# Kernel optimization log

Hardware: AMD Instinct MI355X
Metric: run time of the kernel (lower is better)

## Reference

```python
import jax, jax.numpy as jnp
import numpy as np

VOCAB = 100000
EMBED = 128
HIDDEN = 256
N_TRIPLES = 1_000_000


def setup_inputs() -> dict:
    key = jax.random.key(0)
    ks = jax.random.split(key, 12)

    def xavier(k, fan_in, fan_out):
        limit = float(np.sqrt(6.0 / (fan_in + fan_out)))
        return jax.random.uniform(k, (fan_in, fan_out), jnp.float32, -limit, limit)

    triples = jax.random.randint(ks[0], (N_TRIPLES, 3), 0, VOCAB, dtype=jnp.int32)
    entity_table = jax.random.normal(ks[1], (VOCAB, EMBED), jnp.float32) * 0.02
    relation_table = jax.random.normal(ks[2], (VOCAB, EMBED), jnp.float32) * 0.02
    return {
        "triples": triples,
        "entity_table": entity_table,
        "relation_table": relation_table,
        "W1": xavier(ks[3], 3 * EMBED, HIDDEN), "b1": jnp.zeros((HIDDEN,), jnp.float32),
        "W2": xavier(ks[4], HIDDEN, HIDDEN),    "b2": jnp.zeros((HIDDEN,), jnp.float32),
        "W3": xavier(ks[5], HIDDEN, EMBED),     "b3": jnp.zeros((EMBED,), jnp.float32),
        "Wf1": xavier(ks[6], EMBED, HIDDEN),    "bf1": jnp.zeros((HIDDEN,), jnp.float32),
        "Wf2": xavier(ks[7], HIDDEN, EMBED),    "bf2": jnp.zeros((EMBED,), jnp.float32),
    }


def reference(triples, entity_table, relation_table,
              W1, b1, W2, b2, W3, b3, Wf1, bf1, Wf2, bf2):
    # Batched gather: [N, embed] each
    e1 = entity_table[triples[:, 0]]
    rel = relation_table[triples[:, 1]]
    e2 = entity_table[triples[:, 2]]
    x = jnp.concatenate([e1, rel, e2], axis=-1)  # [N, 3*embed]
    # graph_encoder: Linear-ReLU-Linear-ReLU-Linear
    h = jax.nn.relu(x @ W1 + b1)
    h = jax.nn.relu(h @ W2 + b2)
    enc = h @ W3 + b3                            # [N, embed]
    agg = jnp.mean(enc, axis=0)                  # [embed]
    # final_encoder: Linear-ReLU-Linear
    out = jax.nn.relu(agg @ Wf1 + bf1) @ Wf2 + bf2
    return out
```

## Files before the change

### kernel.cpp

```cpp
#include <hip/hip_runtime.h>
#include <hip/hip_bf16.h>


#define EMBED 128
#define BM 64
#define NBUCKET 128

typedef __bf16 bf16x8 __attribute__((ext_vector_type(8)));
typedef __bf16 bf16x4 __attribute__((ext_vector_type(4)));
typedef float f32x4 __attribute__((ext_vector_type(4)));

__global__ void pack_cvt(const float* __restrict__ src, __bf16* __restrict__ dst,
                         int K, int N) {
    int e = blockIdx.x * 256 + threadIdx.x;
    if (e >= K * N) return;
    int j = e & 7;
    int l = (e >> 3) & 63;
    int tile = e >> 9;
    int KT = K >> 5;
    int kt = tile % KT;
    int mt = tile / KT;
    int k = kt * 32 + (l >> 4) * 8 + j;
    int nc = mt * 16 + (l & 15);
    dst[e] = (__bf16)src[k * N + nc];
}

__global__ __launch_bounds__(256, 3) void mlp_main(
    const int* __restrict__ triples,
    const float* __restrict__ ent, const float* __restrict__ rel,
    const __bf16* __restrict__ W1p, const float* __restrict__ b1,
    const __bf16* __restrict__ W2p, const float* __restrict__ b2,
    const __bf16* __restrict__ W3p,
    float* __restrict__ part, int n)
{
    __shared__ unsigned char lds[49152];
    unsigned char* xs  = lds;
    unsigned char* h1s = lds;
    unsigned char* h2s = lds;

    const int tid  = threadIdx.x;
    const int wave = tid >> 6;
    const int lane = tid & 63;
    const int l15  = lane & 15;
    const int l4   = lane >> 4;
    const int s0   = blockIdx.x * BM;
    const int sp   = tid >> 4;
    const int ch   = tid & 15;

    int rows[3][4];
#pragma unroll
    for (int p = 0; p < 4; p++) {
        int g = s0 + p * 16 + sp;
        const int* t = triples + (g < n ? g : 0) * 3;
        rows[0][p] = t[0]; rows[1][p] = t[1]; rows[2][p] = t[2];
    }
    float4 ga[3][4], gb[3][4];
#pragma unroll
    for (int c = 0; c < 3; c++) {
        const float* tbl = (c == 1) ? rel : ent;
#pragma unroll
        for (int p = 0; p < 4; p++) {
            const float* src = tbl + (long)rows[c][p] * EMBED + ch * 8;
            ga[c][p] = *(const float4*)src;
            gb[c][p] = *(const float4*)(src + 4);
        }
    }
#pragma unroll
    for (int c = 0; c < 3; c++)
#pragma unroll
        for (int p = 0; p < 4; p++) {
            bf16x8 w;
            w[0] = (__bf16)ga[c][p].x; w[1] = (__bf16)ga[c][p].y;
            w[2] = (__bf16)ga[c][p].z; w[3] = (__bf16)ga[c][p].w;
            w[4] = (__bf16)gb[c][p].x; w[5] = (__bf16)gb[c][p].y;
            w[6] = (__bf16)gb[c][p].z; w[7] = (__bf16)gb[c][p].w;
            int s = p * 16 + sp;
            int off = (s * 768 + c * 256 + ch * 16) ^ ((s & 7) << 4);
            *(bf16x8*)(xs + off) = w;
        }
    __syncthreads();

    f32x4 acc[4][4];
    {
        const int fb = wave * 64;
#pragma unroll
        for (int m = 0; m < 4; m++) {
            f32x4 bias = *(const f32x4*)(b1 + fb + m * 16 + l4 * 4);
#pragma unroll
            for (int nn = 0; nn < 4; nn++) acc[m][nn] = bias;
        }
    }
    __builtin_amdgcn_s_setprio(1);
#pragma unroll
    for (int kk = 0; kk < 12; kk++) {
        bf16x8 bfr[4];
#pragma unroll
        for (int nn = 0; nn < 4; nn++) {
            int s = nn * 16 + l15;
            int off = (s * 768 + kk * 64 + l4 * 16) ^ ((s & 7) << 4);
            bfr[nn] = *(const bf16x8*)(xs + off);
        }
        bf16x8 afr[4];
#pragma unroll
        for (int m = 0; m < 4; m++)
            afr[m] = *(const bf16x8*)(W1p + ((wave * 4 + m) * 12 + kk) * 512 + lane * 8);
#pragma unroll
        for (int m = 0; m < 4; m++)
#pragma unroll
            for (int nn = 0; nn < 4; nn++)
                acc[m][nn] = __builtin_amdgcn_mfma_f32_16x16x32_bf16(
                    afr[m], bfr[nn], acc[m][nn], 0, 0, 0);
    }
    __builtin_amdgcn_s_setprio(0);
    __syncthreads();
#pragma unroll
    for (int m = 0; m < 4; m++) {
        int f0 = wave * 64 + m * 16 + l4 * 4;
#pragma unroll
        for (int nn = 0; nn < 4; nn++) {
            int s = nn * 16 + l15;
            bf16x4 p;
#pragma unroll
            for (int j = 0; j < 4; j++) {
                float v = acc[m][nn][j];
                p[j] = (__bf16)(v > 0.f ? v : 0.f);
            }
            int off = (s * 512 + f0 * 2) ^ ((s & 7) << 4);
            *(bf16x4*)(h1s + off) = p;
        }
    }
    __syncthreads();

    f32x4 acc2[4][4];
    {
        const int fb = wave * 64;
#pragma unroll
        for (int m = 0; m < 4; m++) {
            f32x4 bias = *(const f32x4*)(b2 + fb + m * 16 + l4 * 4);
#pragma unroll
            for (int nn = 0; nn < 4; nn++) acc2[m][nn] = bias;
        }
    }
    __builtin_amdgcn_s_setprio(1);
#pragma unroll
    for (int kk = 0; kk < 8; kk++) {
        bf16x8 bfr[4];
#pragma unroll
        for (int nn = 0; nn < 4; nn++) {
            int s = nn * 16 + l15;
            int off = (s * 512 + kk * 64 + l4 * 16) ^ ((s & 7) << 4);
            bfr[nn] = *(const bf16x8*)(h1s + off);
        }
        bf16x8 afr[4];
#pragma unroll
        for (int m = 0; m < 4; m++)
            afr[m] = *(const bf16x8*)(W2p + ((wave * 4 + m) * 8 + kk) * 512 + lane * 8);
#pragma unroll
        for (int m = 0; m < 4; m++)
#pragma unroll
            for (int nn = 0; nn < 4; nn++)
                acc2[m][nn] = __builtin_amdgcn_mfma_f32_16x16x32_bf16(
                    afr[m], bfr[nn], acc2[m][nn], 0, 0, 0);
    }
    __builtin_amdgcn_s_setprio(0);
    __syncthreads();
#pragma unroll
    for (int m = 0; m < 4; m++) {
        int f0 = wave * 64 + m * 16 + l4 * 4;
#pragma unroll
        for (int nn = 0; nn < 4; nn++) {
            int s = nn * 16 + l15;
            bf16x4 p;
#pragma unroll
            for (int j = 0; j < 4; j++) {
                float v = acc2[m][nn][j];
                p[j] = (__bf16)(v > 0.f ? v : 0.f);
            }
            int off = (s * 512 + f0 * 2) ^ ((s & 7) << 4);
            *(bf16x4*)(h2s + off) = p;
        }
    }
    __syncthreads();

    f32x4 acc3[2][4];
#pragma unroll
    for (int m = 0; m < 2; m++)
#pragma unroll
        for (int nn = 0; nn < 4; nn++)
            acc3[m][nn] = (f32x4)(0.f);
    __builtin_amdgcn_s_setprio(1);
#pragma unroll
    for (int kk = 0; kk < 8; kk++) {
        bf16x8 bfr[4];
#pragma unroll
        for (int nn = 0; nn < 4; nn++) {
            int s = nn * 16 + l15;
            int off = (s * 512 + kk * 64 + l4 * 16) ^ ((s & 7) << 4);
            bfr[nn] = *(const bf16x8*)(h2s + off);
        }
        bf16x8 afr[2];
#pragma unroll
        for (int m = 0; m < 2; m++)
            afr[m] = *(const bf16x8*)(W3p + ((wave * 2 + m) * 8 + kk) * 512 + lane * 8);
#pragma unroll
        for (int m = 0; m < 2; m++)
#pragma unroll
            for (int nn = 0; nn < 4; nn++)
                acc3[m][nn] = __builtin_amdgcn_mfma_f32_16x16x32_bf16(
                    afr[m], bfr[nn], acc3[m][nn], 0, 0, 0);
    }
    __builtin_amdgcn_s_setprio(0);
    {
        float* bucket = part + (blockIdx.x & (NBUCKET - 1)) * 128;
#pragma unroll
        for (int m = 0; m < 2; m++) {
#pragma unroll
            for (int j = 0; j < 4; j++) {
                float v = 0.f;
#pragma unroll
                for (int nn = 0; nn < 4; nn++) {
                    int g = s0 + nn * 16 + l15;
                    float t = acc3[m][nn][j];
                    v += (g < n) ? t : 0.f;
                }
                for (int off = 1; off < 16; off <<= 1) v += __shfl_xor(v, off);
                if (l15 == 0) {
                    int f = wave * 32 + m * 16 + l4 * 4 + j;
                    atomicAdd(bucket + f, v);
                }
            }
        }
    }
}

__global__ void head_kernel(const float* __restrict__ part, const float* __restrict__ b3,
                            const float* __restrict__ Wf1, const float* __restrict__ bf1,
                            const float* __restrict__ Wf2, const float* __restrict__ bf2,
                            float* __restrict__ out, int n)
{
    __shared__ float agg[128];
    __shared__ float t[256];
    const int tid = threadIdx.x;
    if (tid < 128) {
        float s = 0.f;
        for (int b = 0; b < NBUCKET; b++) s += part[b * 128 + tid];
        agg[tid] = s / (float)n + b3[tid];
    }
    __syncthreads();
    {
        float a = bf1[tid];
        for (int k = 0; k < 128; k++) a += agg[k] * Wf1[k * 256 + tid];
        t[tid] = a > 0.f ? a : 0.f;
    }
    __syncthreads();
    if (tid < 128) {
        float o = bf2[tid];
        for (int i = 0; i < 256; i++) o += t[i] * Wf2[i * 128 + tid];
        out[tid] = o;
    }
}

extern "C" void kernel_launch(void* const* d_in, const int* in_sizes, int n_in,
                              void* d_out, int out_size, void* d_ws, size_t ws_size,
                              hipStream_t stream) {
    const int*   triples = (const int*)d_in[0];
    const float* ent     = (const float*)d_in[1];
    const float* rel     = (const float*)d_in[2];
    const float* W1      = (const float*)d_in[3];
    const float* b1      = (const float*)d_in[4];
    const float* W2      = (const float*)d_in[5];
    const float* b2      = (const float*)d_in[6];
    const float* W3      = (const float*)d_in[7];
    const float* b3      = (const float*)d_in[8];
    const float* Wf1     = (const float*)d_in[9];
    const float* bf1     = (const float*)d_in[10];
    const float* Wf2     = (const float*)d_in[11];
    const float* bf2     = (const float*)d_in[12];
    float* out = (float*)d_out;
    const int n = in_sizes[0] / 3;

    __bf16* W1p = (__bf16*)d_ws;
    __bf16* W2p = (__bf16*)((char*)d_ws + 196608);
    __bf16* W3p = (__bf16*)((char*)d_ws + 327680);
    float*  prt = (float*)((char*)d_ws + 393216);

    pack_cvt<<<(384 * 256 + 255) / 256, 256, 0, stream>>>(W1, W1p, 384, 256);
    pack_cvt<<<(256 * 256 + 255) / 256, 256, 0, stream>>>(W2, W2p, 256, 256);
    pack_cvt<<<(256 * 128 + 255) / 256, 256, 0, stream>>>(W3, W3p, 256, 128);
    hipMemsetAsync(prt, 0, NBUCKET * 128 * sizeof(float), stream);

    const int blocks = (n + BM - 1) / BM;
    mlp_main<<<blocks, 256, 0, stream>>>(triples, ent, rel, W1p, b1, W2p, b2, W3p, prt, n);
    head_kernel<<<1, 256, 0, stream>>>(prt, b3, Wf1, bf1, Wf2, bf2, out, n);
}
```

Measured before the change: 508.2 us.

## Switch MLP GEMMs to 32x32x16 MFMA and fuse weight prep launches

Replaces the 16x16x32 bf16 MFMA tiling in all three encoder layers with 32x32x16 MFMA tiles. The weight packing layout, accumulator layout, bias initialisation, ReLU writeback and final reduction are all reworked to match. The three pack kernels and the memset are merged into a single prep launch. The larger MFMA tiles need fewer LDS fragment loads per FLOP, at the cost of different register pressure and reduction shuffles.

```diff
diff --git a/kernel.cpp b/kernel.cpp
--- a/kernel.cpp
+++ b/kernel.cpp
@@ -9,19 +9,24 @@
 typedef __bf16 bf16x8 __attribute__((ext_vector_type(8)));
 typedef __bf16 bf16x4 __attribute__((ext_vector_type(4)));
 typedef float f32x4 __attribute__((ext_vector_type(4)));
-
-__global__ void pack_cvt(const float* __restrict__ src, __bf16* __restrict__ dst,
-                         int K, int N) {
-    int e = blockIdx.x * 256 + threadIdx.x;
-    if (e >= K * N) return;
-    int j = e & 7;
-    int l = (e >> 3) & 63;
-    int tile = e >> 9;
-    int KT = K >> 5;
-    int kt = tile % KT;
-    int mt = tile / KT;
-    int k = kt * 32 + (l >> 4) * 8 + j;
-    int nc = mt * 16 + (l & 15);
+typedef float f32x16 __attribute__((ext_vector_type(16)));
+
+__global__ void prep_all(const float* __restrict__ W1, const float* __restrict__ W2,
+                         const float* __restrict__ W3,
+                         __bf16* __restrict__ W1p, __bf16* __restrict__ W2p,
+                         __bf16* __restrict__ W3p, float* __restrict__ prt) {
+    int idx = blockIdx.x * 256 + threadIdx.x;
+    if (idx < NBUCKET * 128) prt[idx] = 0.f;
+    const float* src; __bf16* dst; int K, N, e;
+    if (idx < 98304)       { src = W1; dst = W1p; K = 384; N = 256; e = idx; }
+    else if (idx < 163840) { src = W2; dst = W2p; K = 256; N = 256; e = idx - 98304; }
+    else if (idx < 196608) { src = W3; dst = W3p; K = 256; N = 128; e = idx - 163840; }
+    else return;
+    int j = e & 7, l = (e >> 3) & 63, t = e >> 9;
+    int KT = K >> 4;
+    int kt = t % KT, mt = t / KT;
+    int k  = kt * 16 + (l >> 5) * 8 + j;
+    int nc = mt * 32 + (l & 31);
     dst[e] = (__bf16)src[k * N + nc];
 }
 
@@ -41,8 +46,9 @@
     const int tid  = threadIdx.x;
     const int wave = tid >> 6;
     const int lane = tid & 63;
-    const int l15  = lane & 15;
-    const int l4   = lane >> 4;
+    const int l31  = lane & 31;
+    const int hi   = lane >> 5;
+    const int swzB = (l31 & 7) << 4;
     const int s0   = blockIdx.x * BM;
     const int sp   = tid >> 4;
     const int ch   = tid & 15;
@@ -80,154 +86,147 @@
         }
     __syncthreads();
 
-    f32x4 acc[4][4];
-    {
-        const int fb = wave * 64;
-#pragma unroll
-        for (int m = 0; m < 4; m++) {
-            f32x4 bias = *(const f32x4*)(b1 + fb + m * 16 + l4 * 4);
-#pragma unroll
-            for (int nn = 0; nn < 4; nn++) acc[m][nn] = bias;
-        }
-    }
+    f32x16 acc[2][2];
+#pragma unroll
+    for (int m = 0; m < 2; m++)
+#pragma unroll
+        for (int g = 0; g < 4; g++) {
+            f32x4 bb = *(const f32x4*)(b1 + wave * 64 + m * 32 + g * 8 + hi * 4);
+#pragma unroll
+            for (int nn = 0; nn < 2; nn++)
+#pragma unroll
+                for (int j = 0; j < 4; j++) acc[m][nn][g * 4 + j] = bb[j];
+        }
     __builtin_amdgcn_s_setprio(1);
 #pragma unroll
-    for (int kk = 0; kk < 12; kk++) {
-        bf16x8 bfr[4];
-#pragma unroll
-        for (int nn = 0; nn < 4; nn++) {
-            int s = nn * 16 + l15;
-            int off = (s * 768 + kk * 64 + l4 * 16) ^ ((s & 7) << 4);
-            bfr[nn] = *(const bf16x8*)(xs + off);
-        }
-        bf16x8 afr[4];
-#pragma unroll
-        for (int m = 0; m < 4; m++)
-            afr[m] = *(const bf16x8*)(W1p + ((wave * 4 + m) * 12 + kk) * 512 + lane * 8);
-#pragma unroll
-        for (int m = 0; m < 4; m++)
-#pragma unroll
-            for (int nn = 0; nn < 4; nn++)
-                acc[m][nn] = __builtin_amdgcn_mfma_f32_16x16x32_bf16(
+    for (int kk = 0; kk < 24; kk++) {
+        bf16x8 bfr[2];
+#pragma unroll
+        for (int nn = 0; nn < 2; nn++) {
+            int s = nn * 32 + l31;
+            bfr[nn] = *(const bf16x8*)(xs + ((s * 768 + kk * 32 + hi * 16) ^ swzB));
+        }
+        bf16x8 afr[2];
+#pragma unroll
+        for (int m = 0; m < 2; m++)
+            afr[m] = *(const bf16x8*)(W1p + ((wave * 2 + m) * 24 + kk) * 512 + lane * 8);
+#pragma unroll
+        for (int m = 0; m < 2; m++)
+#pragma unroll
+            for (int nn = 0; nn < 2; nn++)
+                acc[m][nn] = __builtin_amdgcn_mfma_f32_32x32x16_bf16(
                     afr[m], bfr[nn], acc[m][nn], 0, 0, 0);
     }
     __builtin_amdgcn_s_setprio(0);
     __syncthreads();
 #pragma unroll
-    for (int m = 0; m < 4; m++) {
-        int f0 = wave * 64 + m * 16 + l4 * 4;
-#pragma unroll
-        for (int nn = 0; nn < 4; nn++) {
-            int s = nn * 16 + l15;
-            bf16x4 p;
-#pragma unroll
-            for (int j = 0; j < 4; j++) {
-                float v = acc[m][nn][j];
-                p[j] = (__bf16)(v > 0.f ? v : 0.f);
-            }
-            int off = (s * 512 + f0 * 2) ^ ((s & 7) << 4);
-            *(bf16x4*)(h1s + off) = p;
-        }
-    }
-    __syncthreads();
-
-    f32x4 acc2[4][4];
-    {
-        const int fb = wave * 64;
-#pragma unroll
-        for (int m = 0; m < 4; m++) {
-            f32x4 bias = *(const f32x4*)(b2 + fb + m * 16 + l4 * 4);
-#pragma unroll
-            for (int nn = 0; nn < 4; nn++) acc2[m][nn] = bias;
-        }
-    }
+    for (int m = 0; m < 2; m++)
+#pragma unroll
+        for (int nn = 0; nn < 2; nn++) {
+            int s = nn * 32 + l31;
+#pragma unroll
+            for (int g = 0; g < 4; g++) {
+                int f0 = wave * 64 + m * 32 + g * 8 + hi * 4;
+                bf16x4 p;
+#pragma unroll
+                for (int j = 0; j < 4; j++) {
+                    float v = acc[m][nn][g * 4 + j];
+                    p[j] = (__bf16)(v > 0.f ? v : 0.f);
+                }
+                *(bf16x4*)(h1s + ((s * 512 + f0 * 2) ^ ((s & 7) << 4))) = p;
+            }
+        }
+    __syncthreads();
+
+    f32x16 acc2[2][2];
+#pragma unroll
+    for (int m = 0; m < 2; m++)
+#pragma unroll
+        for (int g = 0; g < 4; g++) {
+            f32x4 bb = *(const f32x4*)(b2 + wave * 64 + m * 32 + g * 8 + hi * 4);
+#pragma unroll
+            for (int nn = 0; nn < 2; nn++)
+#pragma unroll
+                for (int j = 0; j < 4; j++) acc2[m][nn][g * 4 + j] = bb[j];
+        }
     __builtin_amdgcn_s_setprio(1);
 #pragma unroll
-    for (int kk = 0; kk < 8; kk++) {
-        bf16x8 bfr[4];
-#pragma unroll
-        for (int nn = 0; nn < 4; nn++) {
-            int s = nn * 16 + l15;
-            int off = (s * 512 + kk * 64 + l4 * 16) ^ ((s & 7) << 4);
-            bfr[nn] = *(const bf16x8*)(h1s + off);
-        }
-        bf16x8 afr[4];
-#pragma unroll
-        for (int m = 0; m < 4; m++)
-            afr[m] = *(const bf16x8*)(W2p + ((wave * 4 + m) * 8 + kk) * 512 + lane * 8);
-#pragma unroll
-        for (int m = 0; m < 4; m++)
-#pragma unroll
-            for (int nn = 0; nn < 4; nn++)
-                acc2[m][nn] = __builtin_amdgcn_mfma_f32_16x16x32_bf16(
+    for (int kk = 0; kk < 16; kk++) {
+        bf16x8 bfr[2];
+#pragma unroll
+        for (int nn = 0; nn < 2; nn++) {
+            int s = nn * 32 + l31;
+            bfr[nn] = *(const bf16x8*)(h1s + ((s * 512 + kk * 32 + hi * 16) ^ swzB));
+        }
+        bf16x8 afr[2];
+#pragma unroll
+        for (int m = 0; m < 2; m++)
+            afr[m] = *(const bf16x8*)(W2p + ((wave * 2 + m) * 16 + kk) * 512 + lane * 8);
+#pragma unroll
+        for (int m = 0; m < 2; m++)
+#pragma unroll
+            for (int nn = 0; nn < 2; nn++)
+                acc2[m][nn] = __builtin_amdgcn_mfma_f32_32x32x16_bf16(
                     afr[m], bfr[nn], acc2[m][nn], 0, 0, 0);
     }
     __builtin_amdgcn_s_setprio(0);
     __syncthreads();
 #pragma unroll
-    for (int m = 0; m < 4; m++) {
-        int f0 = wave * 64 + m * 16 + l4 * 4;
-#pragma unroll
-        for (int nn = 0; nn < 4; nn++) {
-            int s = nn * 16 + l15;
-            bf16x4 p;
-#pragma unroll
-            for (int j = 0; j < 4; j++) {
-                float v = acc2[m][nn][j];
-                p[j] = (__bf16)(v > 0.f ? v : 0.f);
-            }
-            int off = (s * 512 + f0 * 2) ^ ((s & 7) << 4);
-            *(bf16x4*)(h2s + off) = p;
-        }
-    }
-    __syncthreads();
-
-    f32x4 acc3[2][4];
-#pragma unroll
-    for (int m = 0; m < 2; m++)
-#pragma unroll
-        for (int nn = 0; nn < 4; nn++)
-            acc3[m][nn] = (f32x4)(0.f);
+    for (int m = 0; m < 2; m++)
+#pragma unroll
+        for (int nn = 0; nn < 2; nn++) {
+            int s = nn * 32 + l31;
+#pragma unroll
+            for (int g = 0; g < 4; g++) {
+                int f0 = wave * 64 + m * 32 + g * 8 + hi * 4;
+                bf16x4 p;
+#pragma unroll
+                for (int j = 0; j < 4; j++) {
+                    float v = acc2[m][nn][g * 4 + j];
+                    p[j] = (__bf16)(v > 0.f ? v : 0.f);
+                }
+                *(bf16x4*)(h2s + ((s * 512 + f0 * 2) ^ ((s & 7) << 4))) = p;
+            }
+        }
+    __syncthreads();
+
+    f32x16 acc3[2];
+#pragma unroll
+    for (int nn = 0; nn < 2; nn++)
+#pragma unroll
+        for (int j = 0; j < 16; j++) acc3[nn][j] = 0.f;
     __builtin_amdgcn_s_setprio(1);
 #pragma unroll
-    for (int kk = 0; kk < 8; kk++) {
-        bf16x8 bfr[4];
-#pragma unroll
-        for (int nn = 0; nn < 4; nn++) {
-            int s = nn * 16 + l15;
-            int off = (s * 512 + kk * 64 + l4 * 16) ^ ((s & 7) << 4);
-            bfr[nn] = *(const bf16x8*)(h2s + off);
-        }
-        bf16x8 afr[2];
-#pragma unroll
-        for (int m = 0; m < 2; m++)
-            afr[m] = *(const bf16x8*)(W3p + ((wave * 2 + m) * 8 + kk) * 512 + lane * 8);
-#pragma unroll
-        for (int m = 0; m < 2; m++)
-#pragma unroll
-            for (int nn = 0; nn < 4; nn++)
-                acc3[m][nn] = __builtin_amdgcn_mfma_f32_16x16x32_bf16(
-                    afr[m], bfr[nn], acc3[m][nn], 0, 0, 0);
+    for (int kk = 0; kk < 16; kk++) {
+        bf16x8 afr = *(const bf16x8*)(W3p + (wave * 16 + kk) * 512 + lane * 8);
+#pragma unroll
+        for (int nn = 0; nn < 2; nn++) {
+            int s = nn * 32 + l31;
+            bf16x8 bfr = *(const bf16x8*)(h2s + ((s * 512 + kk * 32 + hi * 16) ^ swzB));
+            acc3[nn] = __builtin_amdgcn_mfma_f32_32x32x16_bf16(
+                afr, bfr, acc3[nn], 0, 0, 0);
+        }
     }
     __builtin_amdgcn_s_setprio(0);
     {
         float* bucket = part + (blockIdx.x & (NBUCKET - 1)) * 128;
 #pragma unroll
-        for (int m = 0; m < 2; m++) {
-#pragma unroll
-            for (int j = 0; j < 4; j++) {
-                float v = 0.f;
-#pragma unroll
-                for (int nn = 0; nn < 4; nn++) {
-                    int g = s0 + nn * 16 + l15;
-                    float t = acc3[m][nn][j];
-                    v += (g < n) ? t : 0.f;
-                }
-                for (int off = 1; off < 16; off <<= 1) v += __shfl_xor(v, off);
-                if (l15 == 0) {
-                    int f = wave * 32 + m * 16 + l4 * 4 + j;
-                    atomicAdd(bucket + f, v);
-                }
+        for (int r = 0; r < 16; r++) {
+            float v = 0.f;
+#pragma unroll
+            for (int nn = 0; nn < 2; nn++) {
+                int g = s0 + nn * 32 + l31;
+                float t = acc3[nn][r];
+                v += (g < n) ? t : 0.f;
+            }
+            v += __shfl_xor(v, 1);
+            v += __shfl_xor(v, 2);
+            v += __shfl_xor(v, 4);
+            v += __shfl_xor(v, 8);
+            v += __shfl_xor(v, 16);
+            if (l31 == 0) {
+                int f = wave * 32 + (r & 3) + 8 * (r >> 2) + hi * 4;
+                atomicAdd(bucket + f, v);
             }
         }
     }
@@ -284,10 +283,7 @@
     __bf16* W3p = (__bf16*)((char*)d_ws + 327680);
     float*  prt = (float*)((char*)d_ws + 393216);
 
-    pack_cvt<<<(384 * 256 + 255) / 256, 256, 0, stream>>>(W1, W1p, 384, 256);
-    pack_cvt<<<(256 * 256 + 255) / 256, 256, 0, stream>>>(W2, W2p, 256, 256);
-    pack_cvt<<<(256 * 128 + 255) / 256, 256, 0, stream>>>(W3, W3p, 256, 128);
-    hipMemsetAsync(prt, 0, NBUCKET * 128 * sizeof(float), stream);
+    prep_all<<<768, 256, 0, stream>>>(W1, W2, W3, W1p, W2p, W3p, prt);
 
     const int blocks = (n + BM - 1) / BM;
     mlp_main<<<blocks, 256, 0, stream>>>(triples, ent, rel, W1p, b1, W2p, b2, W3p, prt, n);
```

After: 539.2 us. 6.1% more time.

## Split layer-1 K loop to shrink LDS and merge weight prep launches

Applied to the files above, without the earlier changes.

The X tile in LDS drops from 48KB to 32KB by staging only e1 and rel first. The e2 gather is issued into registers during the first 8 K-steps, then written over the e1 region for the last 4 K-steps. This lets launch bounds rise from 3 to 4 blocks per CU. Separately, the three weight pack kernels and the memset are merged into one prep launch to cut launch overhead. The cost is an extra barrier pair, plus extra live registers for the prefetched gather under a tighter register budget.

```diff
diff --git a/kernel.cpp b/kernel.cpp
--- a/kernel.cpp
+++ b/kernel.cpp
@@ -10,22 +10,26 @@
 typedef __bf16 bf16x4 __attribute__((ext_vector_type(4)));
 typedef float f32x4 __attribute__((ext_vector_type(4)));
 
-__global__ void pack_cvt(const float* __restrict__ src, __bf16* __restrict__ dst,
-                         int K, int N) {
-    int e = blockIdx.x * 256 + threadIdx.x;
-    if (e >= K * N) return;
-    int j = e & 7;
-    int l = (e >> 3) & 63;
-    int tile = e >> 9;
+__global__ void prep_all(const float* __restrict__ W1, const float* __restrict__ W2,
+                         const float* __restrict__ W3,
+                         __bf16* __restrict__ W1p, __bf16* __restrict__ W2p,
+                         __bf16* __restrict__ W3p, float* __restrict__ prt) {
+    int idx = blockIdx.x * 256 + threadIdx.x;
+    if (idx < NBUCKET * 128) prt[idx] = 0.f;
+    const float* src; __bf16* dst; int K, N, e;
+    if (idx < 98304)       { src = W1; dst = W1p; K = 384; N = 256; e = idx; }
+    else if (idx < 163840) { src = W2; dst = W2p; K = 256; N = 256; e = idx - 98304; }
+    else if (idx < 196608) { src = W3; dst = W3p; K = 256; N = 128; e = idx - 163840; }
+    else return;
+    int j = e & 7, l = (e >> 3) & 63, t = e >> 9;
     int KT = K >> 5;
-    int kt = tile % KT;
-    int mt = tile / KT;
-    int k = kt * 32 + (l >> 4) * 8 + j;
+    int kt = t % KT, mt = t / KT;
+    int k  = kt * 32 + (l >> 4) * 8 + j;
     int nc = mt * 16 + (l & 15);
     dst[e] = (__bf16)src[k * N + nc];
 }
 
-__global__ __launch_bounds__(256, 3) void mlp_main(
+__global__ __launch_bounds__(256, 4) void mlp_main(
     const int* __restrict__ triples,
     const float* __restrict__ ent, const float* __restrict__ rel,
     const __bf16* __restrict__ W1p, const float* __restrict__ b1,
@@ -33,8 +37,7 @@
     const __bf16* __restrict__ W3p,
     float* __restrict__ part, int n)
 {
-    __shared__ unsigned char lds[49152];
-    unsigned char* xs  = lds;
+    __shared__ unsigned char lds[32768];
     unsigned char* h1s = lds;
     unsigned char* h2s = lds;
 
@@ -54,9 +57,9 @@
         const int* t = triples + (g < n ? g : 0) * 3;
         rows[0][p] = t[0]; rows[1][p] = t[1]; rows[2][p] = t[2];
     }
-    float4 ga[3][4], gb[3][4];
-#pragma unroll
-    for (int c = 0; c < 3; c++) {
+    float4 ga[2][4], gb[2][4];
+#pragma unroll
+    for (int c = 0; c < 2; c++) {
         const float* tbl = (c == 1) ? rel : ent;
 #pragma unroll
         for (int p = 0; p < 4; p++) {
@@ -66,7 +69,7 @@
         }
     }
 #pragma unroll
-    for (int c = 0; c < 3; c++)
+    for (int c = 0; c < 2; c++)
 #pragma unroll
         for (int p = 0; p < 4; p++) {
             bf16x8 w;
@@ -75,10 +78,18 @@
             w[4] = (__bf16)gb[c][p].x; w[5] = (__bf16)gb[c][p].y;
             w[6] = (__bf16)gb[c][p].z; w[7] = (__bf16)gb[c][p].w;
             int s = p * 16 + sp;
-            int off = (s * 768 + c * 256 + ch * 16) ^ ((s & 7) << 4);
-            *(bf16x8*)(xs + off) = w;
-        }
-    __syncthreads();
+            int off = c * 16384 + ((s * 256 + ch * 16) ^ ((s & 7) << 4));
+            *(bf16x8*)(lds + off) = w;
+        }
+    __syncthreads();
+
+    float4 g2a[4], g2b[4];
+#pragma unroll
+    for (int p = 0; p < 4; p++) {
+        const float* src = ent + (long)rows[2][p] * EMBED + ch * 8;
+        g2a[p] = *(const float4*)src;
+        g2b[p] = *(const float4*)(src + 4);
+    }
 
     f32x4 acc[4][4];
     {
@@ -92,13 +103,49 @@
     }
     __builtin_amdgcn_s_setprio(1);
 #pragma unroll
-    for (int kk = 0; kk < 12; kk++) {
+    for (int kk = 0; kk < 8; kk++) {
         bf16x8 bfr[4];
 #pragma unroll
         for (int nn = 0; nn < 4; nn++) {
             int s = nn * 16 + l15;
-            int off = (s * 768 + kk * 64 + l4 * 16) ^ ((s & 7) << 4);
-            bfr[nn] = *(const bf16x8*)(xs + off);
+            int off = (kk >> 2) * 16384 +
+                      ((s * 256 + (kk & 3) * 64 + l4 * 16) ^ ((s & 7) << 4));
+            bfr[nn] = *(const bf16x8*)(lds + off);
+        }
+        bf16x8 afr[4];
+#pragma unroll
+        for (int m = 0; m < 4; m++)
+            afr[m] = *(const bf16x8*)(W1p + ((wave * 4 + m) * 12 + kk) * 512 + lane * 8);
+#pragma unroll
+        for (int m = 0; m < 4; m++)
+#pragma unroll
+            for (int nn = 0; nn < 4; nn++)
+                acc[m][nn] = __builtin_amdgcn_mfma_f32_16x16x32_bf16(
+                    afr[m], bfr[nn], acc[m][nn], 0, 0, 0);
+    }
+    __builtin_amdgcn_s_setprio(0);
+    __syncthreads();
+#pragma unroll
+    for (int p = 0; p < 4; p++) {
+        bf16x8 w;
+        w[0] = (__bf16)g2a[p].x; w[1] = (__bf16)g2a[p].y;
+        w[2] = (__bf16)g2a[p].z; w[3] = (__bf16)g2a[p].w;
+        w[4] = (__bf16)g2b[p].x; w[5] = (__bf16)g2b[p].y;
+        w[6] = (__bf16)g2b[p].z; w[7] = (__bf16)g2b[p].w;
+        int s = p * 16 + sp;
+        int off = (s * 256 + ch * 16) ^ ((s & 7) << 4);
+        *(bf16x8*)(lds + off) = w;
+    }
+    __syncthreads();
+    __builtin_amdgcn_s_setprio(1);
+#pragma unroll
+    for (int kk = 8; kk < 12; kk++) {
+        bf16x8 bfr[4];
+#pragma unroll
+        for (int nn = 0; nn < 4; nn++) {
+            int s = nn * 16 + l15;
+            int off = (s * 256 + (kk & 3) * 64 + l4 * 16) ^ ((s & 7) << 4);
+            bfr[nn] = *(const bf16x8*)(lds + off);
         }
         bf16x8 afr[4];
 #pragma unroll
@@ -284,10 +331,7 @@
     __bf16* W3p = (__bf16*)((char*)d_ws + 327680);
     float*  prt = (float*)((char*)d_ws + 393216);
 
-    pack_cvt<<<(384 * 256 + 255) / 256, 256, 0, stream>>>(W1, W1p, 384, 256);
-    pack_cvt<<<(256 * 256 + 255) / 256, 256, 0, stream>>>(W2, W2p, 256, 256);
-    pack_cvt<<<(256 * 128 + 255) / 256, 256, 0, stream>>>(W3, W3p, 256, 128);
-    hipMemsetAsync(prt, 0, NBUCKET * 128 * sizeof(float), stream);
+    prep_all<<<768, 256, 0, stream>>>(W1, W2, W3, W1p, W2p, W3p, prt);
 
     const int blocks = (n + BM - 1) / BM;
     mlp_main<<<blocks, 256, 0, stream>>>(triples, ent, rel, W1p, b1, W2p, b2, W3p, prt, n);
```

After: 862.1 us. 69.6% more time.

## Split MLP block work across 8 waves and fuse weight-prep launches

Applied to the files above, without the earlier changes.

Doubles the mlp_main block to 512 threads (8 waves), so each wave computes half as many output-feature tiles per layer. The gather is restructured so each thread loads one row segment of 16 floats per table. The three weight pack kernels and the memset are merged into a single prep kernel to cut launch overhead. The goal is more waves in flight to hide gather latency and lower per-wave register pressure. The cost is that each B fragment read from LDS is now reused by fewer MFMAs, which raises LDS traffic per flop.

```diff
diff --git a/kernel.cpp b/kernel.cpp
--- a/kernel.cpp
+++ b/kernel.cpp
@@ -10,22 +10,26 @@
 typedef __bf16 bf16x4 __attribute__((ext_vector_type(4)));
 typedef float f32x4 __attribute__((ext_vector_type(4)));
 
-__global__ void pack_cvt(const float* __restrict__ src, __bf16* __restrict__ dst,
-                         int K, int N) {
-    int e = blockIdx.x * 256 + threadIdx.x;
-    if (e >= K * N) return;
-    int j = e & 7;
-    int l = (e >> 3) & 63;
-    int tile = e >> 9;
+__global__ void prep_all(const float* __restrict__ W1, const float* __restrict__ W2,
+                         const float* __restrict__ W3,
+                         __bf16* __restrict__ W1p, __bf16* __restrict__ W2p,
+                         __bf16* __restrict__ W3p, float* __restrict__ prt) {
+    int idx = blockIdx.x * 256 + threadIdx.x;
+    if (idx < NBUCKET * 128) prt[idx] = 0.f;
+    const float* src; __bf16* dst; int K, N, e;
+    if (idx < 98304)       { src = W1; dst = W1p; K = 384; N = 256; e = idx; }
+    else if (idx < 163840) { src = W2; dst = W2p; K = 256; N = 256; e = idx - 98304; }
+    else if (idx < 196608) { src = W3; dst = W3p; K = 256; N = 128; e = idx - 163840; }
+    else return;
+    int j = e & 7, l = (e >> 3) & 63, t = e >> 9;
     int KT = K >> 5;
-    int kt = tile % KT;
-    int mt = tile / KT;
-    int k = kt * 32 + (l >> 4) * 8 + j;
+    int kt = t % KT, mt = t / KT;
+    int k  = kt * 32 + (l >> 4) * 8 + j;
     int nc = mt * 16 + (l & 15);
     dst[e] = (__bf16)src[k * N + nc];
 }
 
-__global__ __launch_bounds__(256, 3) void mlp_main(
+__global__ __launch_bounds__(512, 6) void mlp_main(
     const int* __restrict__ triples,
     const float* __restrict__ ent, const float* __restrict__ rel,
     const __bf16* __restrict__ W1p, const float* __restrict__ b1,
@@ -44,51 +48,43 @@
     const int l15  = lane & 15;
     const int l4   = lane >> 4;
     const int s0   = blockIdx.x * BM;
-    const int sp   = tid >> 4;
-    const int ch   = tid & 15;
-
-    int rows[3][4];
-#pragma unroll
-    for (int p = 0; p < 4; p++) {
-        int g = s0 + p * 16 + sp;
-        const int* t = triples + (g < n ? g : 0) * 3;
-        rows[0][p] = t[0]; rows[1][p] = t[1]; rows[2][p] = t[2];
-    }
-    float4 ga[3][4], gb[3][4];
-#pragma unroll
-    for (int c = 0; c < 3; c++) {
-        const float* tbl = (c == 1) ? rel : ent;
-#pragma unroll
-        for (int p = 0; p < 4; p++) {
-            const float* src = tbl + (long)rows[c][p] * EMBED + ch * 8;
-            ga[c][p] = *(const float4*)src;
-            gb[c][p] = *(const float4*)(src + 4);
-        }
-    }
-#pragma unroll
-    for (int c = 0; c < 3; c++)
-#pragma unroll
-        for (int p = 0; p < 4; p++) {
-            bf16x8 w;
-            w[0] = (__bf16)ga[c][p].x; w[1] = (__bf16)ga[c][p].y;
-            w[2] = (__bf16)ga[c][p].z; w[3] = (__bf16)ga[c][p].w;
-            w[4] = (__bf16)gb[c][p].x; w[5] = (__bf16)gb[c][p].y;
-            w[6] = (__bf16)gb[c][p].z; w[7] = (__bf16)gb[c][p].w;
-            int s = p * 16 + sp;
-            int off = (s * 768 + c * 256 + ch * 16) ^ ((s & 7) << 4);
-            *(bf16x8*)(xs + off) = w;
-        }
-    __syncthreads();
-
-    f32x4 acc[4][4];
+    const int sg   = tid >> 3;
+    const int q    = tid & 7;
+
     {
-        const int fb = wave * 64;
-#pragma unroll
-        for (int m = 0; m < 4; m++) {
-            f32x4 bias = *(const f32x4*)(b1 + fb + m * 16 + l4 * 4);
-#pragma unroll
-            for (int nn = 0; nn < 4; nn++) acc[m][nn] = bias;
-        }
+        int g = s0 + sg;
+        const int* tp = triples + (g < n ? g : 0) * 3;
+#pragma unroll
+        for (int c = 0; c < 3; c++) {
+            const float* tbl = (c == 1) ? rel : ent;
+            const float* src = tbl + (long)tp[c] * EMBED + q * 16;
+            float4 v0 = *(const float4*)(src);
+            float4 v1 = *(const float4*)(src + 4);
+            float4 v2 = *(const float4*)(src + 8);
+            float4 v3 = *(const float4*)(src + 12);
+            bf16x8 w0, w1;
+            w0[0] = (__bf16)v0.x; w0[1] = (__bf16)v0.y;
+            w0[2] = (__bf16)v0.z; w0[3] = (__bf16)v0.w;
+            w0[4] = (__bf16)v1.x; w0[5] = (__bf16)v1.y;
+            w0[6] = (__bf16)v1.z; w0[7] = (__bf16)v1.w;
+            w1[0] = (__bf16)v2.x; w1[1] = (__bf16)v2.y;
+            w1[2] = (__bf16)v2.z; w1[3] = (__bf16)v2.w;
+            w1[4] = (__bf16)v3.x; w1[5] = (__bf16)v3.y;
+            w1[6] = (__bf16)v3.z; w1[7] = (__bf16)v3.w;
+            int base = sg * 768 + c * 256 + q * 32;
+            int swz  = (sg & 7) << 4;
+            *(bf16x8*)(xs + (base ^ swz))        = w0;
+            *(bf16x8*)(xs + ((base + 16) ^ swz)) = w1;
+        }
+    }
+    __syncthreads();
+
+    f32x4 acc[2][4];
+#pragma unroll
+    for (int m = 0; m < 2; m++) {
+        f32x4 bias = *(const f32x4*)(b1 + wave * 32 + m * 16 + l4 * 4);
+#pragma unroll
+        for (int nn = 0; nn < 4; nn++) acc[m][nn] = bias;
     }
     __builtin_amdgcn_s_setprio(1);
 #pragma unroll
@@ -100,12 +96,12 @@
             int off = (s * 768 + kk * 64 + l4 * 16) ^ ((s & 7) << 4);
             bfr[nn] = *(const bf16x8*)(xs + off);
         }
-        bf16x8 afr[4];
-#pragma unroll
-        for (int m = 0; m < 4; m++)
-            afr[m] = *(const bf16x8*)(W1p + ((wave * 4 + m) * 12 + kk) * 512 + lane * 8);
-#pragma unroll
-        for (int m = 0; m < 4; m++)
+        bf16x8 afr[2];
+#pragma unroll
+        for (int m = 0; m < 2; m++)
+            afr[m] = *(const bf16x8*)(W1p + ((wave * 2 + m) * 12 + kk) * 512 + lane * 8);
+#pragma unroll
+        for (int m = 0; m < 2; m++)
 #pragma unroll
             for (int nn = 0; nn < 4; nn++)
                 acc[m][nn] = __builtin_amdgcn_mfma_f32_16x16x32_bf16(
@@ -114,8 +110,8 @@
     __builtin_amdgcn_s_setprio(0);
     __syncthreads();
 #pragma unroll
-    for (int m = 0; m < 4; m++) {
-        int f0 = wave * 64 + m * 16 + l4 * 4;
+    for (int m = 0; m < 2; m++) {
+        int f0 = wave * 32 + m * 16 + l4 * 4;
 #pragma unroll
         for (int nn = 0; nn < 4; nn++) {
             int s = nn * 16 + l15;
@@ -131,15 +127,12 @@
     }
     __syncthreads();
 
-    f32x4 acc2[4][4];
-    {
-        const int fb = wave * 64;
-#pragma unroll
-        for (int m = 0; m < 4; m++) {
-            f32x4 bias = *(const f32x4*)(b2 + fb + m * 16 + l4 * 4);
-#pragma unroll
-            for (int nn = 0; nn < 4; nn++) acc2[m][nn] = bias;
-        }
+    f32x4 acc2[2][4];
+#pragma unroll
+    for (int m = 0; m < 2; m++) {
+        f32x4 bias = *(const f32x4*)(b2 + wave * 32 + m * 16 + l4 * 4);
+#pragma unroll
+        for (int nn = 0; nn < 4; nn++) acc2[m][nn] = bias;
     }
     __builtin_amdgcn_s_setprio(1);
 #pragma unroll
@@ -151,12 +144,12 @@
             int off = (s * 512 + kk * 64 + l4 * 16) ^ ((s & 7) << 4);
             bfr[nn] = *(const bf16x8*)(h1s + off);
         }
-        bf16x8 afr[4];
-#pragma unroll
-        for (int m = 0; m < 4; m++)
-            afr[m] = *(const bf16x8*)(W2p + ((wave * 4 + m) * 8 + kk) * 512 + lane * 8);
-#pragma unroll
-        for (int m = 0; m < 4; m++)
+        bf16x8 afr[2];
+#pragma unroll
+        for (int m = 0; m < 2; m++)
+            afr[m] = *(const bf16x8*)(W2p + ((wave * 2 + m) * 8 + kk) * 512 + lane * 8);
+#pragma unroll
+        for (int m = 0; m < 2; m++)
 #pragma unroll
             for (int nn = 0; nn < 4; nn++)
                 acc2[m][nn] = __builtin_amdgcn_mfma_f32_16x16x32_bf16(
@@ -165,8 +158,8 @@
     __builtin_amdgcn_s_setprio(0);
     __syncthreads();
 #pragma unroll
-    for (int m = 0; m < 4; m++) {
-        int f0 = wave * 64 + m * 16 + l4 * 4;
+    for (int m = 0; m < 2; m++) {
+        int f0 = wave * 32 + m * 16 + l4 * 4;
 #pragma unroll
         for (int nn = 0; nn < 4; nn++) {
             int s = nn * 16 + l15;
@@ -182,52 +175,38 @@
     }
     __syncthreads();
 
-    f32x4 acc3[2][4];
-#pragma unroll
-    for (int m = 0; m < 2; m++)
-#pragma unroll
-        for (int nn = 0; nn < 4; nn++)
-            acc3[m][nn] = (f32x4)(0.f);
+    f32x4 acc3[4];
+#pragma unroll
+    for (int nn = 0; nn < 4; nn++) acc3[nn] = (f32x4)(0.f);
     __builtin_amdgcn_s_setprio(1);
 #pragma unroll
     for (int kk = 0; kk < 8; kk++) {
-        bf16x8 bfr[4];
+        bf16x8 afr = *(const bf16x8*)(W3p + (wave * 8 + kk) * 512 + lane * 8);
 #pragma unroll
         for (int nn = 0; nn < 4; nn++) {
             int s = nn * 16 + l15;
             int off = (s * 512 + kk * 64 + l4 * 16) ^ ((s & 7) << 4);
-            bfr[nn] = *(const bf16x8*)(h2s + off);
-        }
-        bf16x8 afr[2];
-#pragma unroll
-        for (int m = 0; m < 2; m++)
-            afr[m] = *(const bf16x8*)(W3p + ((wave * 2 + m) * 8 + kk) * 512 + lane * 8);
-#pragma unroll
-        for (int m = 0; m < 2; m++)
-#pragma unroll
-            for (int nn = 0; nn < 4; nn++)
-                acc3[m][nn] = __builtin_amdgcn_mfma_f32_16x16x32_bf16(
-                    afr[m], bfr[nn], acc3[m][nn], 0, 0, 0);
+            bf16x8 bfr = *(const bf16x8*)(h2s + off);
+            acc3[nn] = __builtin_amdgcn_mfma_f32_16x16x32_bf16(
+                afr, bfr, acc3[nn], 0, 0, 0);
+        }
     }
     __builtin_amdgcn_s_setprio(0);
     {
         float* bucket = part + (blockIdx.x & (NBUCKET - 1)) * 128;
 #pragma unroll
-        for (int m = 0; m < 2; m++) {
-#pragma unroll
-            for (int j = 0; j < 4; j++) {
-                float v = 0.f;
-#pragma unroll
-                for (int nn = 0; nn < 4; nn++) {
-                    int g = s0 + nn * 16 + l15;
-                    float t = acc3[m][nn][j];
-                    v += (g < n) ? t : 0.f;
-                }
-                for (int off = 1; off < 16; off <<= 1) v += __shfl_xor(v, off);
-                if (l15 == 0) {
-                    int f = wave * 32 + m * 16 + l4 * 4 + j;
-                    atomicAdd(bucket + f, v);
-                }
+        for (int j = 0; j < 4; j++) {
+            float v = 0.f;
+#pragma unroll
+            for (int nn = 0; nn < 4; nn++) {
+                int g = s0 + nn * 16 + l15;
+                float t = acc3[nn][j];
+                v += (g < n) ? t : 0.f;
+            }
+            for (int off = 1; off < 16; off <<= 1) v += __shfl_xor(v, off);
+            if (l15 == 0) {
+                int f = wave * 16 + l4 * 4 + j;
+                atomicAdd(bucket + f, v);
             }
         }
     }
@@ -284,12 +263,9 @@
     __bf16* W3p = (__bf16*)((char*)d_ws + 327680);
     float*  prt = (float*)((char*)d_ws + 393216);
 
-    pack_cvt<<<(384 * 256 + 255) / 256, 256, 0, stream>>>(W1, W1p, 384, 256);
-    pack_cvt<<<(256 * 256 + 255) / 256, 256, 0, stream>>>(W2, W2p, 256, 256);
-    pack_cvt<<<(256 * 128 + 255) / 256, 256, 0, stream>>>(W3, W3p, 256, 128);
-    hipMemsetAsync(prt, 0, NBUCKET * 128 * sizeof(float), stream);
+    prep_all<<<768, 256, 0, stream>>>(W1, W2, W3, W1p, W2p, W3p, prt);
 
     const int blocks = (n + BM - 1) / BM;
-    mlp_main<<<blocks, 256, 0, stream>>>(triples, ent, rel, W1p, b1, W2p, b2, W3p, prt, n);
+    mlp_main<<<blocks, 512, 0, stream>>>(triples, ent, rel, W1p, b1, W2p, b2, W3p, prt, n);
     head_kernel<<<1, 256, 0, stream>>>(prt, b3, Wf1, bf1, Wf2, bf2, out, n);
 }
```

Result: slower. 665.3 us (+30.9%).
